# Performance work log

Hardware: AMD Instinct MI355X
Metric: run time of the kernel (lower is better)

Reference implementation:

```python
import jax, jax.numpy as jnp
import numpy as np

B, N, D = 32, 4096, 256      # batch, num input features, input dim
S, H, M = 11, 256, 512       # num_slots, slot_size, mlp_hidden_size
ITERS = 3
ATTN_EPS = 1e-8
LN_EPS = 1e-5


def layer_norm(x, scale, offset):
    mu = jnp.mean(x, axis=-1, keepdims=True)
    var = jnp.var(x, axis=-1, keepdims=True)
    return (x - mu) * scale * jax.lax.rsqrt(var + LN_EPS) + offset


def gru_unroll(updates, w_i, w_h, b):
    # haiku hk.GRU unrolled over axis 1 (time_major=False), zero initial state.
    # updates: [B, T, H]
    h0 = jnp.zeros((updates.shape[0], H), updates.dtype)
    def step(h, x):
        gx = jnp.matmul(x, w_i)                                    # [B, 3H]
        zr = jax.nn.sigmoid(gx[:, :2 * H] + jnp.matmul(h, w_h[:, :2 * H]) + b[:2 * H])
        z, r = zr[:, :H], zr[:, H:]
        a = jnp.tanh(gx[:, 2 * H:] + jnp.matmul(r * h, w_h[:, 2 * H:]) + b[2 * H:])
        h_new = (1.0 - z) * h + z * a
        return h_new, h_new
    _, outs = jax.lax.scan(step, h0, jnp.swapaxes(updates, 0, 1))
    return jnp.swapaxes(outs, 0, 1)                                # [B, T, H]


def setup_inputs():
    key = jax.random.key(0)
    k = jax.random.split(key, 16)
    def lin(kk, fan_in, fan_out):
        return jax.random.normal(kk, (fan_in, fan_out), jnp.float32) / np.sqrt(fan_in).astype(np.float32)
    return {
        "inputs": jax.random.normal(k[0], (B, N, D), jnp.float32),
        "slot_noise": jax.random.normal(k[1], (B, S, H), jnp.float32),
        "ln_in_scale": jnp.ones((D,), jnp.float32),
        "ln_in_offset": jnp.zeros((D,), jnp.float32),
        "ln_slots_scale": jnp.ones((H,), jnp.float32),
        "ln_slots_offset": jnp.zeros((H,), jnp.float32),
        "ln_mlp_scale": jnp.ones((H,), jnp.float32),
        "ln_mlp_offset": jnp.zeros((H,), jnp.float32),
        "slots_mu": jax.random.normal(k[2], (1, 1, H), jnp.float32) * 0.1,
        "slots_log_sigma": jax.random.normal(k[3], (1, 1, H), jnp.float32) * 0.1 - 1.0,
        "Wq": lin(k[4], H, H),
        "Wk": lin(k[5], D, H),
        "Wv": lin(k[6], D, H),
        "gru_wi": lin(k[7], H, 3 * H),
        "gru_wh": lin(k[8], H, 3 * H),
        "gru_b": jnp.zeros((3 * H,), jnp.float32),
        "mlp_w1": lin(k[9], H, M),
        "mlp_b1": jnp.zeros((M,), jnp.float32),
        "mlp_w2": lin(k[10], M, H),
        "mlp_b2": jnp.zeros((H,), jnp.float32),
    }


def reference(inputs, slot_noise, ln_in_scale, ln_in_offset, ln_slots_scale,
              ln_slots_offset, ln_mlp_scale, ln_mlp_offset, slots_mu,
              slots_log_sigma, Wq, Wk, Wv, gru_wi, gru_wh, gru_b,
              mlp_w1, mlp_b1, mlp_w2, mlp_b2):
    x = layer_norm(inputs, ln_in_scale, ln_in_offset)
    kf = jnp.matmul(x, Wk)                                          # [B, N, H]
    vf = jnp.matmul(x, Wv)                                          # [B, N, H]
    slots = slots_mu + jnp.exp(slots_log_sigma) * slot_noise        # [B, S, H]
    scale = H ** (-0.5)
    for _ in range(ITERS):
        q = jnp.matmul(layer_norm(slots, ln_slots_scale, ln_slots_offset), Wq) * scale
        attn_logits = jnp.einsum('bnh,bsh->bns', kf, q)             # [B, N, S]
        attn = jax.nn.softmax(attn_logits, axis=-1) + ATTN_EPS      # softmax over slots
        attn = attn / jnp.sum(attn, axis=-2, keepdims=True)         # normalize over inputs
        updates = jnp.einsum('bns,bnh->bsh', attn, vf)              # [B, S, H]
        slots = gru_unroll(updates, gru_wi, gru_wh, gru_b)          # GRU over slot axis
        mlp_in = layer_norm(slots, ln_mlp_scale, ln_mlp_offset)
        hid = jax.nn.relu(jnp.matmul(mlp_in, mlp_w1) + mlp_b1)
        slots = slots + jnp.matmul(hid, mlp_w2) + mlp_b2
    return slots
```

## Files before the change

kernel.cpp:

```cpp
#include <hip/hip_runtime.h>

typedef unsigned short u16;
typedef __bf16 bf16x8 __attribute__((ext_vector_type(8)));
typedef float  f32x4  __attribute__((ext_vector_type(4)));
typedef unsigned short u16x8 __attribute__((ext_vector_type(8)));

union U8cast { u16x8 u; bf16x8 b; };

#define NB 32
#define NN 4096
#define ND 256
#define NS 11
#define NH 256
#define NM 512

__device__ __forceinline__ u16 f2bf(float f) {
  unsigned u = __float_as_uint(f);
  u += 0x7FFF + ((u >> 16) & 1);
  return (u16)(u >> 16);
}
__device__ __forceinline__ float bf2f(u16 h) {
  return __uint_as_float(((unsigned)h) << 16);
}

__global__ void k_stats_ln(const float* __restrict__ x, const float* __restrict__ sc,
                           const float* __restrict__ of, u16* __restrict__ xbf) {
  int lane = threadIdx.x & 63;
  int wid  = threadIdx.x >> 6;
  int row  = blockIdx.x * 4 + wid;
  float4 v = *(const float4*)(x + (size_t)row * 256 + lane * 4);
  float s1 = v.x + v.y + v.z + v.w;
  float s2 = v.x*v.x + v.y*v.y + v.z*v.z + v.w*v.w;
#pragma unroll
  for (int off = 32; off; off >>= 1) { s1 += __shfl_xor(s1, off); s2 += __shfl_xor(s2, off); }
  float mu = s1 * (1.f/256.f);
  float rs = rsqrtf(s2 * (1.f/256.f) - mu*mu + 1e-5f);
  float4 s4 = *(const float4*)(sc + lane * 4);
  float4 o4 = *(const float4*)(of + lane * 4);
  ushort4 o;
  o.x = f2bf((v.x - mu) * (rs * s4.x) + o4.x);
  o.y = f2bf((v.y - mu) * (rs * s4.y) + o4.y);
  o.z = f2bf((v.z - mu) * (rs * s4.z) + o4.z);
  o.w = f2bf((v.w - mu) * (rs * s4.w) + o4.w);
  *(ushort4*)(xbf + (size_t)row * 256 + lane * 4) = o;
}

__global__ __launch_bounds__(256)
void k_cvt_w(const float* __restrict__ Wk, u16* __restrict__ wT) {
  __shared__ float Lt[64][65];
  int bx = blockIdx.x;
  int kt = bx & 3, ct = bx >> 2;
  int k0 = kt * 64, c0 = ct * 64;
  int t = threadIdx.x;
  int kr = t >> 2, part = t & 3;
  const float* sp = Wk + (size_t)(k0 + kr) * 256 + c0 + part * 16;
#pragma unroll
  for (int g = 0; g < 4; ++g) {
    float4 v = *(const float4*)(sp + g * 4);
    Lt[kr][part*16 + g*4 + 0] = v.x;
    Lt[kr][part*16 + g*4 + 1] = v.y;
    Lt[kr][part*16 + g*4 + 2] = v.z;
    Lt[kr][part*16 + g*4 + 3] = v.w;
  }
  __syncthreads();
  int cr = t >> 2;
  u16* wp = wT + (size_t)(c0 + cr) * 256 + k0 + part * 16;
#pragma unroll
  for (int g = 0; g < 2; ++g) {
    u16x8 o;
#pragma unroll
    for (int j = 0; j < 8; ++j) o[j] = f2bf(Lt[part*16 + g*8 + j][cr]);
    *(u16x8*)(wp + g * 8) = o;
  }
}

__global__ __launch_bounds__(256)
void k_mk(const float* __restrict__ Wq, const u16* __restrict__ wT,
          u16* __restrict__ Mb) {
  __shared__ float xn[256];
  __shared__ float part[8][256];
  int e = blockIdx.x, t = threadIdx.x;
  xn[t] = Wq[e*256 + t];
  __syncthreads();
  int tc = t & 31, kg = t >> 5;
  float a[8] = {};
#pragma unroll 8
  for (int kk = 0; kk < 32; ++kk) {
    int k = kg*32 + kk;
    float xv = xn[k];
    u16x8 wv = *(const u16x8*)(wT + k*256 + tc*8);
#pragma unroll
    for (int j = 0; j < 8; ++j) a[j] += xv * bf2f(wv[j]);
  }
  *(float4*)&part[kg][tc*8]     = make_float4(a[0], a[1], a[2], a[3]);
  *(float4*)&part[kg][tc*8 + 4] = make_float4(a[4], a[5], a[6], a[7]);
  __syncthreads();
  float s = 0.f;
#pragma unroll
  for (int g = 0; g < 8; ++g) s += part[g][t];
  Mb[e*256 + t] = f2bf(s);
}

__global__ __launch_bounds__(384)
void k_wvi(const float* __restrict__ Wv, const float* __restrict__ wi,
           u16* __restrict__ wvib) {
  __shared__ float xn[256];
  __shared__ float part[4][768];
  int d = blockIdx.x, t = threadIdx.x;
  if (t < 256) xn[t] = Wv[d*256 + t];
  __syncthreads();
  int tc = t % 96, kg = t / 96;
  float a[8] = {};
#pragma unroll 4
  for (int kk = 0; kk < 64; ++kk) {
    int k = kg*64 + kk;
    float xv = xn[k];
    float4 w0 = *(const float4*)(wi + (size_t)k*768 + tc*8);
    float4 w1 = *(const float4*)(wi + (size_t)k*768 + tc*8 + 4);
    a[0] += xv * w0.x; a[1] += xv * w0.y; a[2] += xv * w0.z; a[3] += xv * w0.w;
    a[4] += xv * w1.x; a[5] += xv * w1.y; a[6] += xv * w1.z; a[7] += xv * w1.w;
  }
  *(float4*)&part[kg][tc*8]     = make_float4(a[0], a[1], a[2], a[3]);
  *(float4*)&part[kg][tc*8 + 4] = make_float4(a[4], a[5], a[6], a[7]);
  __syncthreads();
#pragma unroll
  for (int c = t; c < 768; c += 384) {
    float s = part[0][c] + part[1][c] + part[2][c] + part[3][c];
    wvib[d*768 + c] = f2bf(s);
  }
}

__global__ void k_cvt_all(const float* __restrict__ wh, const float* __restrict__ w1,
                          const float* __restrict__ w2,
                          const float* __restrict__ noise, const float* __restrict__ smu,
                          const float* __restrict__ sls,
                          u16* __restrict__ whb, u16* __restrict__ w1b,
                          u16* __restrict__ w2b, float* __restrict__ slots) {
  int idx = blockIdx.x * 256 + threadIdx.x;
  if      (idx < 196608) whb[idx]          = f2bf(wh[idx]);
  else if (idx < 327680) w1b[idx - 196608] = f2bf(w1[idx - 196608]);
  else if (idx < 458752) w2b[idx - 327680] = f2bf(w2[idx - 327680]);
  else {
    int i = idx - 458752;
    int c = i & 255;
    slots[i] = smu[c] + expf(sls[c]) * noise[i];
  }
}

__global__ __launch_bounds__(256)
void k_q_ln(const float* __restrict__ slots, const float* __restrict__ sc,
            const float* __restrict__ of, const u16* __restrict__ Mb,
            float* __restrict__ qk2) {
  __shared__ float xn[256];
  __shared__ float red[8];
  __shared__ float part[8][256];
  int row = blockIdx.x, t = threadIdx.x;
  float v = slots[row*256 + t];
  float s1 = v, s2 = v*v;
#pragma unroll
  for (int off = 32; off; off >>= 1) { s1 += __shfl_xor(s1, off); s2 += __shfl_xor(s2, off); }
  int w = t >> 6;
  if ((t & 63) == 0) { red[w*2] = s1; red[w*2+1] = s2; }
  __syncthreads();
  float a1 = red[0] + red[2] + red[4] + red[6];
  float a2 = red[1] + red[3] + red[5] + red[7];
  float mu = a1 * (1.f/256.f);
  float rs = rsqrtf(a2 * (1.f/256.f) - mu*mu + 1e-5f);
  xn[t] = (v - mu) * rs * sc[t] + of[t];
  __syncthreads();
  int tc = t & 31, kg = t >> 5;
  float a[8] = {};
#pragma unroll 8
  for (int kk = 0; kk < 32; ++kk) {
    int k = kg*32 + kk;
    float xv = xn[k];
    u16x8 wv = *(const u16x8*)(Mb + k*256 + tc*8);
#pragma unroll
    for (int j = 0; j < 8; ++j) a[j] += xv * bf2f(wv[j]);
  }
  *(float4*)&part[kg][tc*8]     = make_float4(a[0], a[1], a[2], a[3]);
  *(float4*)&part[kg][tc*8 + 4] = make_float4(a[4], a[5], a[6], a[7]);
  __syncthreads();
  float s = 0.f;
#pragma unroll
  for (int g = 0; g < 8; ++g) s += part[g][t];
  qk2[row*256 + t] = s * 0.0625f;
}

__global__ __launch_bounds__(256)
void k_attn_up(const u16* __restrict__ xbf, const float* __restrict__ qg,
               float* __restrict__ upart, float* __restrict__ cpart) {
  __shared__ __align__(16) u16 vfL[64][256];
  __shared__ __align__(16) u16 qTL[16][264];
  __shared__ __align__(16) u16 PTL[16][72];
  __shared__ float Lg[64][17];
  __shared__ float csw[4][12];
  int t = threadIdx.x;
  int b = blockIdx.y;
  int bx = blockIdx.x;
  int nb0 = bx * 256;
  int lane = t & 63, w = t >> 6;
  int fr = lane & 15, kq = lane >> 4;

#pragma unroll
  for (int i = t; i < 512; i += 256) {
    int s = i >> 5, k0 = (i & 31) * 8;
    u16x8 o;
    if (s < 11) {
      const float* qp = qg + (size_t)b*2816 + s*256 + k0;
#pragma unroll
      for (int j = 0; j < 8; ++j) o[j] = f2bf(qp[j]);
    } else {
#pragma unroll
      for (int j = 0; j < 8; ++j) o[j] = 0;
    }
    *(u16x8*)&qTL[s][k0] = o;
  }
  for (int i = t; i < 16*72; i += 256) ((u16*)PTL)[i] = 0;

  f32x4 accU[4] = {};
  float cs0 = 0.f, cs1 = 0.f, cs2 = 0.f;
  int rS = t >> 2, g4 = t & 3;
  int j32  = t & 31;
  int nsub = t >> 5;
  int js   = (j32 ^ nsub) * 8;
  int hc   = j32 * 8;

  for (int c = 0; c < 4; ++c) {
    int n0 = nb0 + c*64;
    __syncthreads();
    {
#pragma unroll
      for (int nr = 0; nr < 8; ++nr) {
        int n = nr*8 + nsub;
        size_t base = ((size_t)b*4096 + n0 + n) * 256;
        u16x8 kvk = *(const u16x8*)(xbf + base + hc);
        *(u16x8*)&vfL[n][js] = kvk;
      }
    }
    __syncthreads();
    {
      f32x4 aL = {};
      int n = w*16 + fr;
#pragma unroll
      for (int kc = 0; kc < 256; kc += 32) {
        bf16x8 af = *(const bf16x8*)&vfL[n][((kc/8 + kq) ^ (fr & 7)) * 8];
        bf16x8 bq = *(const bf16x8*)&qTL[fr][kc + kq*8];
        aL = __builtin_amdgcn_mfma_f32_16x16x32_bf16(af, bq, aL, 0, 0, 0);
      }
#pragma unroll
      for (int r = 0; r < 4; ++r)
        Lg[w*16 + kq*4 + r][fr] = aL[r];
    }
    __syncthreads();
    {
      float p0 = Lg[rS][g4];
      float p1 = Lg[rS][g4 + 4];
      float p2 = (g4 < 3) ? Lg[rS][g4 + 8] : -1e30f;
      float m = fmaxf(fmaxf(p0, p1), p2);
      m = fmaxf(m, __shfl_xor(m, 1));
      m = fmaxf(m, __shfl_xor(m, 2));
      p0 = __expf(p0 - m); p1 = __expf(p1 - m);
      p2 = (g4 < 3) ? __expf(p2 - m) : 0.f;
      float Z = p0 + p1 + p2;
      Z += __shfl_xor(Z, 1);
      Z += __shfl_xor(Z, 2);
      float iz = 1.f / Z;
      u16 b0 = f2bf(p0*iz + 1e-8f);
      u16 b1 = f2bf(p1*iz + 1e-8f);
      PTL[g4][rS]     = b0;  cs0 += bf2f(b0);
      PTL[g4 + 4][rS] = b1;  cs1 += bf2f(b1);
      if (g4 < 3) {
        u16 b2 = f2bf(p2*iz + 1e-8f);
        PTL[g4 + 8][rS] = b2;  cs2 += bf2f(b2);
      }
    }
    __syncthreads();
#pragma unroll
    for (int ht = 0; ht < 4; ++ht) {
      int h = w*64 + ht*16 + fr;
      int h3 = h >> 3, h7 = h & 7;
#pragma unroll
      for (int kc = 0; kc < 64; kc += 32) {
        bf16x8 aP = *(const bf16x8*)&PTL[fr][kc + kq*8];
        U8cast bv;
#pragma unroll
        for (int j = 0; j < 8; ++j) {
          int k = kc + kq*8 + j;
          bv.u[j] = vfL[k][((h3 ^ j) << 3) | h7];
        }
        accU[ht] = __builtin_amdgcn_mfma_f32_16x16x32_bf16(aP, bv.b, accU[ht], 0, 0, 0);
      }
    }
  }
  {
    size_t ub = ((size_t)bx*352 + (size_t)b*11) * 256;
#pragma unroll
    for (int ht = 0; ht < 4; ++ht) {
      int h = w*64 + ht*16 + fr;
#pragma unroll
      for (int r = 0; r < 4; ++r) {
        int s = kq*4 + r;
        if (s < 11)
          upart[ub + (size_t)s*256 + h] = accU[ht][r];
      }
    }
  }
  {
#pragma unroll
    for (int off = 4; off < 64; off <<= 1) {
      cs0 += __shfl_xor(cs0, off);
      cs1 += __shfl_xor(cs1, off);
      cs2 += __shfl_xor(cs2, off);
    }
    if (lane < 4) { csw[w][lane] = cs0; csw[w][lane + 4] = cs1; }
    if (lane < 3) { csw[w][lane + 8] = cs2; }
    __syncthreads();
    if (t < 11)
      cpart[(size_t)bx*512 + b*16 + t] =
          csw[0][t] + csw[1][t] + csw[2][t] + csw[3][t];
  }
}

__global__ __launch_bounds__(384)
void k_gx(const float* __restrict__ upart, const float* __restrict__ cpart,
          const u16* __restrict__ wvib, float* __restrict__ gx) {
  __shared__ float xn[256];
  __shared__ float part[4][768];
  __shared__ float red16[16];
  int row = blockIdx.x, t = threadIdx.x;
  if (t < 16) red16[t] = cpart[(size_t)t*512 + (row/11)*16 + (row%11)];
  __syncthreads();
  if (t < 256) {
    float cs = 0.f;
#pragma unroll
    for (int p = 0; p < 16; ++p) cs += red16[p];
    float s = 0.f;
#pragma unroll
    for (int p = 0; p < 16; ++p) s += upart[((size_t)p*352 + row)*256 + t];
    xn[t] = s / cs;
  }
  __syncthreads();
  int tc = t % 96, kg = t / 96;
  float a[8] = {};
#pragma unroll 4
  for (int kk = 0; kk < 64; ++kk) {
    int k = kg*64 + kk;
    float xv = xn[k];
    u16x8 wv = *(const u16x8*)(wvib + k*768 + tc*8);
#pragma unroll
    for (int j = 0; j < 8; ++j) a[j] += xv * bf2f(wv[j]);
  }
  *(float4*)&part[kg][tc*8]     = make_float4(a[0], a[1], a[2], a[3]);
  *(float4*)&part[kg][tc*8 + 4] = make_float4(a[4], a[5], a[6], a[7]);
  __syncthreads();
#pragma unroll
  for (int c = t; c < 768; c += 384) {
    float s = part[0][c] + part[1][c] + part[2][c] + part[3][c];
    gx[row*768 + c] = s;
  }
}

__global__ __launch_bounds__(512)
void k_gru(const float* __restrict__ gx, const u16* __restrict__ whb,
           const float* __restrict__ gb, float* __restrict__ slots) {
  __shared__ float h[256], rh[256], zv[256];
  __shared__ float part[4096];
  int b = blockIdx.x, t = threadIdx.x;
  if (t < 256) h[t] = 0.f;
  __syncthreads();
  for (int step = 0; step < 11; ++step) {
    int row = b*11 + step;
    {
      int tc = t & 63, kg = t >> 6;
      float a[8] = {};
#pragma unroll 8
      for (int kk = 0; kk < 32; ++kk) {
        int k = kg*32 + kk;
        float xv = h[k];
        u16x8 wv = *(const u16x8*)(whb + k*768 + tc*8);
#pragma unroll
        for (int j = 0; j < 8; ++j) a[j] += xv * bf2f(wv[j]);
      }
      *(float4*)&part[kg*512 + tc*8]     = make_float4(a[0], a[1], a[2], a[3]);
      *(float4*)&part[kg*512 + tc*8 + 4] = make_float4(a[4], a[5], a[6], a[7]);
    }
    __syncthreads();
    {
      int c = t;
      float s = gx[row*768 + c] + gb[c];
#pragma unroll
      for (int g = 0; g < 8; ++g) s += part[g*512 + c];
      float sg = 1.f / (1.f + __expf(-s));
      if (c < 256) zv[c] = sg;
      else         rh[c - 256] = sg * h[c - 256];
    }
    __syncthreads();
    {
      int tc = t & 31, kg = t >> 5;
      float a[8] = {};
#pragma unroll 8
      for (int kk = 0; kk < 16; ++kk) {
        int k = kg*16 + kk;
        float xv = rh[k];
        u16x8 wv = *(const u16x8*)(whb + k*768 + 512 + tc*8);
#pragma unroll
        for (int j = 0; j < 8; ++j) a[j] += xv * bf2f(wv[j]);
      }
      *(float4*)&part[kg*256 + tc*8]     = make_float4(a[0], a[1], a[2], a[3]);
      *(float4*)&part[kg*256 + tc*8 + 4] = make_float4(a[4], a[5], a[6], a[7]);
    }
    __syncthreads();
    if (t < 256) {
      int c = t;
      float s = gx[row*768 + 512 + c] + gb[512 + c];
#pragma unroll
      for (int g = 0; g < 16; ++g) s += part[g*256 + c];
      float av = tanhf(s);
      float hn = (1.f - zv[c])*h[c] + zv[c]*av;
      h[c] = hn;
      slots[row*256 + c] = hn;
    }
    __syncthreads();
  }
}

__global__ __launch_bounds__(256)
void k_mlp(float* __restrict__ slots, const float* __restrict__ sc,
           const float* __restrict__ of, const u16* __restrict__ w1b,
           const float* __restrict__ b1, const u16* __restrict__ w2b,
           const float* __restrict__ b2,
           const float* __restrict__ sls_, const float* __restrict__ slo,
           const u16* __restrict__ Mb, float* __restrict__ qk2,
           float* __restrict__ out2) {
  __shared__ float xn[256];
  __shared__ float hid[512];
  __shared__ float red[8];
  __shared__ float part[2048];
  int row = blockIdx.x, t = threadIdx.x;
  float v = slots[row*256 + t];
  float s1 = v, s2 = v*v;
#pragma unroll
  for (int off = 32; off; off >>= 1) { s1 += __shfl_xor(s1, off); s2 += __shfl_xor(s2, off); }
  int w = t >> 6;
  if ((t & 63) == 0) { red[w*2] = s1; red[w*2+1] = s2; }
  __syncthreads();
  float a1s = red[0] + red[2] + red[4] + red[6];
  float a2s = red[1] + red[3] + red[5] + red[7];
  float mu = a1s * (1.f/256.f);
  float rs = rsqrtf(a2s * (1.f/256.f) - mu*mu + 1e-5f);
  xn[t] = (v - mu) * rs * sc[t] + of[t];
  __syncthreads();
  {
    int tc = t & 63, kg = t >> 6;
    float a[8] = {};
#pragma unroll 4
    for (int kk = 0; kk < 64; ++kk) {
      int k = kg*64 + kk;
      float xv = xn[k];
      u16x8 wv = *(const u16x8*)(w1b + k*512 + tc*8);
#pragma unroll
      for (int j = 0; j < 8; ++j) a[j] += xv * bf2f(wv[j]);
    }
    *(float4*)&part[kg*512 + tc*8]     = make_float4(a[0], a[1], a[2], a[3]);
    *(float4*)&part[kg*512 + tc*8 + 4] = make_float4(a[4], a[5], a[6], a[7]);
  }
  __syncthreads();
#pragma unroll
  for (int c = t; c < 512; c += 256) {
    float s = b1[c];
#pragma unroll
    for (int g = 0; g < 4; ++g) s += part[g*512 + c];
    hid[c] = fmaxf(s, 0.f);
  }
  __syncthreads();
  {
    int tc = t & 31, kg = t >> 5;
    float a[8] = {};
#pragma unroll 4
    for (int kk = 0; kk < 64; ++kk) {
      int k = kg*64 + kk;
      float xv = hid[k];
      u16x8 wv = *(const u16x8*)(w2b + k*256 + tc*8);
#pragma unroll
      for (int j = 0; j < 8; ++j) a[j] += xv * bf2f(wv[j]);
    }
    *(float4*)&part[kg*256 + tc*8]     = make_float4(a[0], a[1], a[2], a[3]);
    *(float4*)&part[kg*256 + tc*8 + 4] = make_float4(a[4], a[5], a[6], a[7]);
  }
  __syncthreads();
  float snew;
  {
    float s = v + b2[t];
#pragma unroll
    for (int g = 0; g < 8; ++g) s += part[g*256 + t];
    snew = s;
    slots[row*256 + t] = snew;
    if (out2) out2[row*256 + t] = snew;
  }
  if (!qk2) return;
  float q1 = snew, q2 = snew*snew;
#pragma unroll
  for (int off = 32; off; off >>= 1) { q1 += __shfl_xor(q1, off); q2 += __shfl_xor(q2, off); }
  __syncthreads();
  if ((t & 63) == 0) { red[w*2] = q1; red[w*2+1] = q2; }
  __syncthreads();
  {
    float b1v = red[0] + red[2] + red[4] + red[6];
    float b2v = red[1] + red[3] + red[5] + red[7];
    float mu2 = b1v * (1.f/256.f);
    float rs2 = rsqrtf(b2v * (1.f/256.f) - mu2*mu2 + 1e-5f);
    xn[t] = (snew - mu2) * rs2 * sls_[t] + slo[t];
  }
  __syncthreads();
  {
    int tc = t & 31, kg = t >> 5;
    float a[8] = {};
#pragma unroll 8
    for (int kk = 0; kk < 32; ++kk) {
      int k = kg*32 + kk;
      float xv = xn[k];
      u16x8 wv = *(const u16x8*)(Mb + k*256 + tc*8);
#pragma unroll
      for (int j = 0; j < 8; ++j) a[j] += xv * bf2f(wv[j]);
    }
    *(float4*)&part[kg*256 + tc*8]     = make_float4(a[0], a[1], a[2], a[3]);
    *(float4*)&part[kg*256 + tc*8 + 4] = make_float4(a[4], a[5], a[6], a[7]);
  }
  __syncthreads();
  {
    float s = 0.f;
#pragma unroll
    for (int g = 0; g < 8; ++g) s += part[g*256 + t];
    qk2[row*256 + t] = s * 0.0625f;
  }
}

extern "C" void kernel_launch(void* const* d_in, const int* in_sizes, int n_in,
                              void* d_out, int out_size, void* d_ws, size_t ws_size,
                              hipStream_t stream) {
  (void)in_sizes; (void)n_in; (void)out_size; (void)ws_size;
  const float* inputs = (const float*)d_in[0];
  const float* noise  = (const float*)d_in[1];
  const float* lnin_s = (const float*)d_in[2];
  const float* lnin_o = (const float*)d_in[3];
  const float* lnsl_s = (const float*)d_in[4];
  const float* lnsl_o = (const float*)d_in[5];
  const float* lnml_s = (const float*)d_in[6];
  const float* lnml_o = (const float*)d_in[7];
  const float* smu    = (const float*)d_in[8];
  const float* sls    = (const float*)d_in[9];
  const float* Wq     = (const float*)d_in[10];
  const float* Wk     = (const float*)d_in[11];
  const float* Wv     = (const float*)d_in[12];
  const float* gwi    = (const float*)d_in[13];
  const float* gwh    = (const float*)d_in[14];
  const float* gb     = (const float*)d_in[15];
  const float* w1     = (const float*)d_in[16];
  const float* b1     = (const float*)d_in[17];
  const float* w2     = (const float*)d_in[18];
  const float* b2     = (const float*)d_in[19];

  char* ws = (char*)d_ws;
  u16*    wT      = (u16*)(ws + 134217728);
  float*  qk2     = (float*)(ws + 135000064);
  float*  slots   = (float*)(ws + 139984896);
  float*  gx      = (float*)(ws + 140705792);
  u16*    Mb      = (u16*)(ws + 141789184);
  u16*    wvib    = (u16*)(ws + 141920256);
  u16*    whb     = (u16*)(ws + 142313472);
  u16*    w1b     = (u16*)(ws + 142706688);
  u16*    w2b     = (u16*)(ws + 142968832);
  u16*    xbf     = (u16*)(ws + 143230976);
  float*  upart   = (float*)(ws + 210339840);
  float*  cpart   = (float*)(ws + 216107008);

  k_stats_ln <<<32768, 256, 0, stream>>>(inputs, lnin_s, lnin_o, xbf);
  k_cvt_w    <<<16,    256, 0, stream>>>(Wk, wT);
  k_mk       <<<256,   256, 0, stream>>>(Wq, wT, Mb);
  k_wvi      <<<256,   384, 0, stream>>>(Wv, gwi, wvib);
  k_cvt_all  <<<2144,  256, 0, stream>>>(gwh, w1, w2, noise, smu, sls,
                                         whb, w1b, w2b, slots);
  k_q_ln     <<<352,   256, 0, stream>>>(slots, lnsl_s, lnsl_o, Mb, qk2);

  for (int it = 0; it < 3; ++it) {
    k_attn_up <<<dim3(16, 32), 256, 0, stream>>>(xbf, qk2, upart, cpart);
    k_gx      <<<352, 384, 0, stream>>>(upart, cpart, wvib, gx);
    k_gru     <<<32,  512, 0, stream>>>(gx, whb, gb, slots);
    k_mlp     <<<352, 256, 0, stream>>>(slots, lnml_s, lnml_o, w1b, b1, w2b, b2,
                                        lnsl_s, lnsl_o, Mb,
                                        (it < 2) ? qk2 : nullptr,
                                        (it == 2) ? (float*)d_out : nullptr);
  }
}
```

Measured before the change: 528.7 us.

## Process four batch rows per GRU block to reuse recurrent weight loads

The GRU kernel now handles four batch elements per block, so each bf16 weight vector of w_h is loaded and converted once and applied to four hidden states. This cuts global/L2 weight traffic per step by four. In exchange, the grid shrinks from 32 to 8 blocks, leaving most CUs idle. Shared memory grows to about 76 KB and register pressure rises, which may lower occupancy.

Measured after the change: 793.5 us. 50.1% more time.

```diff
diff --git a/kernel.cpp b/kernel.cpp
--- a/kernel.cpp
+++ b/kernel.cpp
@@ -364,62 +364,90 @@
 __global__ __launch_bounds__(512)
 void k_gru(const float* __restrict__ gx, const u16* __restrict__ whb,
            const float* __restrict__ gb, float* __restrict__ slots) {
-  __shared__ float h[256], rh[256], zv[256];
-  __shared__ float part[4096];
-  int b = blockIdx.x, t = threadIdx.x;
-  if (t < 256) h[t] = 0.f;
+  __shared__ float h[4][256], rh[4][256], zv[4][256];
+  __shared__ float part[4][4096];
+  int b0 = blockIdx.x * 4, t = threadIdx.x;
+  if (t < 256) {
+#pragma unroll
+    for (int bb = 0; bb < 4; ++bb) h[bb][t] = 0.f;
+  }
   __syncthreads();
   for (int step = 0; step < 11; ++step) {
-    int row = b*11 + step;
     {
       int tc = t & 63, kg = t >> 6;
-      float a[8] = {};
+      float a[4][8] = {};
 #pragma unroll 8
       for (int kk = 0; kk < 32; ++kk) {
         int k = kg*32 + kk;
-        float xv = h[k];
         u16x8 wv = *(const u16x8*)(whb + k*768 + tc*8);
-#pragma unroll
-        for (int j = 0; j < 8; ++j) a[j] += xv * bf2f(wv[j]);
-      }
-      *(float4*)&part[kg*512 + tc*8]     = make_float4(a[0], a[1], a[2], a[3]);
-      *(float4*)&part[kg*512 + tc*8 + 4] = make_float4(a[4], a[5], a[6], a[7]);
+        float wf[8];
+#pragma unroll
+        for (int j = 0; j < 8; ++j) wf[j] = bf2f(wv[j]);
+#pragma unroll
+        for (int bb = 0; bb < 4; ++bb) {
+          float xv = h[bb][k];
+#pragma unroll
+          for (int j = 0; j < 8; ++j) a[bb][j] += xv * wf[j];
+        }
+      }
+#pragma unroll
+      for (int bb = 0; bb < 4; ++bb) {
+        *(float4*)&part[bb][kg*512 + tc*8]     = make_float4(a[bb][0], a[bb][1], a[bb][2], a[bb][3]);
+        *(float4*)&part[bb][kg*512 + tc*8 + 4] = make_float4(a[bb][4], a[bb][5], a[bb][6], a[bb][7]);
+      }
     }
     __syncthreads();
     {
       int c = t;
-      float s = gx[row*768 + c] + gb[c];
-#pragma unroll
-      for (int g = 0; g < 8; ++g) s += part[g*512 + c];
-      float sg = 1.f / (1.f + __expf(-s));
-      if (c < 256) zv[c] = sg;
-      else         rh[c - 256] = sg * h[c - 256];
+#pragma unroll
+      for (int bb = 0; bb < 4; ++bb) {
+        int row = (b0 + bb)*11 + step;
+        float s = gx[row*768 + c] + gb[c];
+#pragma unroll
+        for (int g = 0; g < 8; ++g) s += part[bb][g*512 + c];
+        float sg = 1.f / (1.f + __expf(-s));
+        if (c < 256) zv[bb][c] = sg;
+        else         rh[bb][c - 256] = sg * h[bb][c - 256];
+      }
     }
     __syncthreads();
     {
       int tc = t & 31, kg = t >> 5;
-      float a[8] = {};
+      float a[4][8] = {};
 #pragma unroll 8
       for (int kk = 0; kk < 16; ++kk) {
         int k = kg*16 + kk;
-        float xv = rh[k];
         u16x8 wv = *(const u16x8*)(whb + k*768 + 512 + tc*8);
-#pragma unroll
-        for (int j = 0; j < 8; ++j) a[j] += xv * bf2f(wv[j]);
-      }
-      *(float4*)&part[kg*256 + tc*8]     = make_float4(a[0], a[1], a[2], a[3]);
-      *(float4*)&part[kg*256 + tc*8 + 4] = make_float4(a[4], a[5], a[6], a[7]);
+        float wf[8];
+#pragma unroll
+        for (int j = 0; j < 8; ++j) wf[j] = bf2f(wv[j]);
+#pragma unroll
+        for (int bb = 0; bb < 4; ++bb) {
+          float xv = rh[bb][k];
+#pragma unroll
+          for (int j = 0; j < 8; ++j) a[bb][j] += xv * wf[j];
+        }
+      }
+#pragma unroll
+      for (int bb = 0; bb < 4; ++bb) {
+        *(float4*)&part[bb][kg*256 + tc*8]     = make_float4(a[bb][0], a[bb][1], a[bb][2], a[bb][3]);
+        *(float4*)&part[bb][kg*256 + tc*8 + 4] = make_float4(a[bb][4], a[bb][5], a[bb][6], a[bb][7]);
+      }
     }
     __syncthreads();
     if (t < 256) {
       int c = t;
-      float s = gx[row*768 + 512 + c] + gb[512 + c];
-#pragma unroll
-      for (int g = 0; g < 16; ++g) s += part[g*256 + c];
-      float av = tanhf(s);
-      float hn = (1.f - zv[c])*h[c] + zv[c]*av;
-      h[c] = hn;
-      slots[row*256 + c] = hn;
+#pragma unroll
+      for (int bb = 0; bb < 4; ++bb) {
+        int row = (b0 + bb)*11 + step;
+        float s = gx[row*768 + 512 + c] + gb[512 + c];
+#pragma unroll
+        for (int g = 0; g < 16; ++g) s += part[bb][g*256 + c];
+        float av = tanhf(s);
+        float hn = (1.f - zv[bb][c])*h[bb][c] + zv[bb][c]*av;
+        h[bb][c] = hn;
+        slots[row*256 + c] = hn;
+      }
     }
     __syncthreads();
   }
@@ -586,7 +614,7 @@
   for (int it = 0; it < 3; ++it) {
     k_attn_up <<<dim3(16, 32), 256, 0, stream>>>(xbf, qk2, upart, cpart);
     k_gx      <<<352, 384, 0, stream>>>(upart, cpart, wvib, gx);
-    k_gru     <<<32,  512, 0, stream>>>(gx, whb, gb, slots);
+    k_gru     <<<8,   512, 0, stream>>>(gx, whb, gb, slots);
     k_mlp     <<<352, 256, 0, stream>>>(slots, lnml_s, lnml_o, w1b, b1, w2b, b2,
                                         lnsl_s, lnsl_o, Mb,
                                         (it < 2) ? qk2 : nullptr,
```
